# Optimization experiments

Hardware: AMD Instinct MI355X
Metric: run time of the kernel (lower is better)

Reference implementation:

```python
import jax, jax.numpy as jnp
import numpy as np

INPUT_DIM, OUTPUT_DIM = 128, 256
FPS_FACTOR, KNN = 14, 10


def fps(pcd, K):
    """Farthest point sampling. pcd: [B,N,3] -> (points [B,K,3], indices [B,K]).
    Deterministic start at index 0 (pytorch3d uses first/random point)."""
    B, N, _ = pcd.shape
    first = jnp.zeros((B,), jnp.int32)
    init_d = jnp.full((B, N), 1e10, pcd.dtype)

    def step(carry, _):
        dists, last = carry
        lp = jnp.take_along_axis(pcd, last[:, None, None], axis=1)  # [B,1,3]
        d = jnp.sum((pcd - lp) ** 2, axis=-1)                        # [B,N]
        dists = jnp.minimum(dists, d)
        nxt = jnp.argmax(dists, axis=-1).astype(jnp.int32)
        return (dists, nxt), nxt

    (_, _), rest = jax.lax.scan(step, (init_d, first), None, length=K - 1)
    idx = jnp.concatenate([first[None, :], rest], axis=0).T  # [B,K]
    pts = jnp.take_along_axis(pcd, idx[..., None], axis=1)   # [B,K,3]
    return pts, idx


def knn_idx(q, p, k):
    """q:[B,Q,3], p:[B,N,3] -> nearest-neighbor indices [B,Q,k] (squared L2)."""
    d = (jnp.sum(q * q, -1)[:, :, None] + jnp.sum(p * p, -1)[:, None, :]
         - 2.0 * jnp.einsum('bqc,bnc->bqn', q, p))
    _, idx = jax.lax.top_k(-d, k)
    return idx


_bgather = jax.vmap(lambda a, i: a[i])  # per-batch fancy gather


def setup_inputs() -> dict:
    key = jax.random.key(0)
    k1, k2, k3, k4, k5 = jax.random.split(key, 5)
    B, N = 4, 16384
    tgt = jax.random.normal(k1, (B, N, INPUT_DIM), jnp.float32)
    pcd_x = jax.random.normal(k2, (B, N, 3), jnp.float32)
    pcd_v = jax.random.normal(k3, (B, N, 3, 3), jnp.float32)
    W = jax.random.normal(k4, (INPUT_DIM, OUTPUT_DIM), jnp.float32) / np.sqrt(INPUT_DIM)
    b = jax.random.normal(k5, (OUTPUT_DIM,), jnp.float32) * 0.01
    return {"tgt": tgt, "pcd_x": pcd_x, "pcd_v": pcd_v, "W": W, "b": b}


def reference(tgt, pcd_x, pcd_v, W, b):
    B, N, D = tgt.shape
    n_out = N // FPS_FACTOR
    out_pcd_x, out_indices = fps(pcd_x, n_out)          # [B,n_out,3], [B,n_out]
    nn = knn_idx(out_pcd_x, pcd_x, KNN)                 # [B,n_out,k]

    knn_pcd = _bgather(pcd_x, nn)                       # [B,n_out,k,3]
    query_f = jnp.take_along_axis(tgt, out_indices[..., None], axis=1)  # [B,n_out,D]
    query_c = out_pcd_x
    query_v = _bgather(pcd_v, out_indices)              # [B,n_out,V,3]
    key_f = _bgather(tgt, nn)                           # [B,n_out,k,D]
    key_c = knn_pcd
    key_v = _bgather(pcd_v, nn)                         # [B,n_out,k,V,3]

    # flatten (B*n_out) super-point groups, project features
    _query_f = query_f.reshape(-1, D)[:, None, :] @ W + b          # [B*n_out,1,O]
    _key_f = key_f.reshape(-1, KNN, D) @ W + b                     # [B*n_out,k,O]
    del _key_f, key_c, key_v  # consumed by the (identity stand-in) transformer

    # NOTE: URSATransformer stand-in = identity on the projected query features
    out_query_f = _query_f.reshape(B, n_out, OUTPUT_DIM)
    return out_query_f, query_c, query_v
```

## Files before the change

### kernel.cpp

```cpp
#include <hip/hip_runtime.h>

constexpr int B_   = 4;
constexpr int N_   = 16384;
constexpr int NOUT = 1170;
constexpr int D_   = 128;
constexpr int O_   = 256;

typedef float f32x2 __attribute__((ext_vector_type(2)));
typedef unsigned long long u64;

template <int CTRL>
__device__ __forceinline__ float dpp_fmax(float x) {
  int yi = __builtin_amdgcn_update_dpp(__float_as_int(x), __float_as_int(x),
                                       CTRL, 0xF, 0xF, false);
  return fmaxf(x, __int_as_float(yi));
}

constexpr int TPB_FPS = 512;
constexpr int PPT   = N_ / TPB_FPS;
constexpr int NPAIR = PPT / 2;
constexpr int NW    = TPB_FPS / 64;

__global__ __launch_bounds__(TPB_FPS)
__attribute__((amdgpu_waves_per_eu(2, 2)))
void fps_kernel(const float* __restrict__ pcd_x,
                int* __restrict__ sel,
                float* __restrict__ out_c) {
  const int b = blockIdx.x, t = threadIdx.x;
  const float* __restrict__ P = pcd_x + (size_t)b * N_ * 3;
  const int base = t * PPT;
  const int lane = t & 63;

  f32x2 x[NPAIR], y[NPAIR], z[NPAIR], dm[NPAIR];
#pragma unroll
  for (int k = 0; k < NPAIR; ++k) {
    const int p0 = base + 2 * k;
    x[k]  = f32x2{P[p0 * 3 + 0], P[p0 * 3 + 3]};
    y[k]  = f32x2{P[p0 * 3 + 1], P[p0 * 3 + 4]};
    z[k]  = f32x2{P[p0 * 3 + 2], P[p0 * 3 + 5]};
    dm[k] = f32x2{1e10f, 1e10f};
  }

  __shared__ float2 s_pair[2][NW];

  float lx = P[0], ly = P[1], lz = P[2];
  if (t == 0) {
    sel[b * NOUT + 0] = 0;
    out_c[((size_t)b * NOUT + 0) * 3 + 0] = lx;
    out_c[((size_t)b * NOUT + 0) * 3 + 1] = ly;
    out_c[((size_t)b * NOUT + 0) * 3 + 2] = lz;
  }

  for (int step = 1; step < NOUT; ++step) {
    const int par = step & 1;

    asm volatile("" : "+v"(x[0]), "+v"(x[1]), "+v"(x[2]), "+v"(x[3]),
                      "+v"(x[4]), "+v"(x[5]), "+v"(x[6]), "+v"(x[7]),
                      "+v"(x[8]), "+v"(x[9]), "+v"(x[10]), "+v"(x[11]),
                      "+v"(x[12]), "+v"(x[13]), "+v"(x[14]), "+v"(x[15]));
    asm volatile("" : "+v"(y[0]), "+v"(y[1]), "+v"(y[2]), "+v"(y[3]),
                      "+v"(y[4]), "+v"(y[5]), "+v"(y[6]), "+v"(y[7]),
                      "+v"(y[8]), "+v"(y[9]), "+v"(y[10]), "+v"(y[11]),
                      "+v"(y[12]), "+v"(y[13]), "+v"(y[14]), "+v"(y[15]));
    asm volatile("" : "+v"(z[0]), "+v"(z[1]), "+v"(z[2]), "+v"(z[3]),
                      "+v"(z[4]), "+v"(z[5]), "+v"(z[6]), "+v"(z[7]),
                      "+v"(z[8]), "+v"(z[9]), "+v"(z[10]), "+v"(z[11]),
                      "+v"(z[12]), "+v"(z[13]), "+v"(z[14]), "+v"(z[15]));

    const f32x2 lxx = {lx, lx}, lyy = {ly, ly}, lzz = {lz, lz};
    f32x2 bv2 = {-1.0f, -1.0f};
    {
#pragma clang fp contract(off)
#pragma unroll
      for (int k = 0; k < NPAIR; ++k) {
        const f32x2 dx = x[k] - lxx;
        const f32x2 dy = y[k] - lyy;
        const f32x2 dz = z[k] - lzz;
        const f32x2 s  = (dx * dx + dy * dy) + dz * dz;
        f32x2 nd;
        nd.x = fminf(dm[k].x, s.x);
        nd.y = fminf(dm[k].y, s.y);
        dm[k] = nd;
        bv2.x = fmaxf(bv2.x, nd.x);
        bv2.y = fmaxf(bv2.y, nd.y);
      }
    }
    const float bv = fmaxf(bv2.x, bv2.y);

    float wm = bv;
    wm = dpp_fmax<0xB1>(wm);
    wm = dpp_fmax<0x4E>(wm);
    wm = dpp_fmax<0x141>(wm);
    wm = dpp_fmax<0x140>(wm);
    wm = dpp_fmax<0x142>(wm);
    wm = dpp_fmax<0x143>(wm);
    const float wmax =
        __int_as_float(__builtin_amdgcn_readlane(__float_as_int(wm), 63));

    int bi = 0;
#pragma unroll
    for (int k = NPAIR - 1; k >= 0; --k) {
      if (dm[k].y == bv) bi = base + 2 * k + 1;
      if (dm[k].x == bv) bi = base + 2 * k;
    }

    const u64 mask = __ballot(bv == wmax);
    const int flane = __builtin_ctzll(mask);
    if (lane == flane) {
      float2 pr;
      pr.x = wmax;
      pr.y = __int_as_float(bi);
      s_pair[par][t >> 6] = pr;
    }
    __syncthreads();

    const float2 e = s_pair[par][lane & (NW - 1)];
    float gv = e.x;
    gv = dpp_fmax<0xB1>(gv);
    gv = dpp_fmax<0x4E>(gv);
    gv = dpp_fmax<0x141>(gv);
    const u64 m2 = __ballot(e.x == gv);
    const int ww = __builtin_ctzll(m2);
    int ri = __builtin_amdgcn_readlane(__float_as_int(e.y), ww);

    lx = P[ri * 3 + 0];
    ly = P[ri * 3 + 1];
    lz = P[ri * 3 + 2];
    if (t == 0) {
      sel[b * NOUT + step] = ri;
      out_c[((size_t)b * NOUT + step) * 3 + 0] = lx;
      out_c[((size_t)b * NOUT + step) * 3 + 1] = ly;
      out_c[((size_t)b * NOUT + step) * 3 + 2] = lz;
    }
  }
}

constexpr int TPB_PROJ = 256;
constexpr int RPB = 4;

__global__ __launch_bounds__(TPB_PROJ)
void proj_kernel(const float* __restrict__ tgt,
                 const float* __restrict__ pcd_v,
                 const float* __restrict__ W,
                 const float* __restrict__ bias,
                 const int* __restrict__ sel,
                 float* __restrict__ out_f,
                 float* __restrict__ out_v) {
  const int t = threadIdx.x;
  const int row0 = blockIdx.x * RPB;
  __shared__ float sA[RPB * D_];
  __shared__ int   sIdx[RPB];
  if (t < RPB) {
    const int row = row0 + t;
    const int b = row / NOUT;
    sIdx[t] = b * N_ + sel[row];
  }
  __syncthreads();
#pragma unroll
  for (int l = 0; l < RPB * D_ / TPB_PROJ; ++l) {
    const int e = t + l * TPB_PROJ;
    const int r = e >> 7, k = e & (D_ - 1);
    sA[e] = tgt[(size_t)sIdx[r] * D_ + k];
  }
  __syncthreads();
  float acc0 = 0.f, acc1 = 0.f, acc2 = 0.f, acc3 = 0.f;
#pragma unroll 8
  for (int k = 0; k < D_; ++k) {
    const float w = W[k * O_ + t];
    acc0 = fmaf(sA[0 * D_ + k], w, acc0);
    acc1 = fmaf(sA[1 * D_ + k], w, acc1);
    acc2 = fmaf(sA[2 * D_ + k], w, acc2);
    acc3 = fmaf(sA[3 * D_ + k], w, acc3);
  }
  const float bb = bias[t];
  out_f[(size_t)(row0 + 0) * O_ + t] = acc0 + bb;
  out_f[(size_t)(row0 + 1) * O_ + t] = acc1 + bb;
  out_f[(size_t)(row0 + 2) * O_ + t] = acc2 + bb;
  out_f[(size_t)(row0 + 3) * O_ + t] = acc3 + bb;
  if (t < RPB * 9) {
    const int r = t / 9, e = t - r * 9;
    out_v[(size_t)(row0 + r) * 9 + e] = pcd_v[(size_t)sIdx[r] * 9 + e];
  }
}

extern "C" void kernel_launch(void* const* d_in, const int* in_sizes, int n_in,
                              void* d_out, int out_size, void* d_ws, size_t ws_size,
                              hipStream_t stream) {
  const float* tgt   = (const float*)d_in[0];
  const float* pcd_x = (const float*)d_in[1];
  const float* pcd_v = (const float*)d_in[2];
  const float* W     = (const float*)d_in[3];
  const float* bias  = (const float*)d_in[4];

  float* out   = (float*)d_out;
  float* out_f = out;
  float* out_c = out + (size_t)B_ * NOUT * O_;
  float* out_v = out_c + (size_t)B_ * NOUT * 3;

  int* sel = (int*)d_ws;

  hipLaunchKernelGGL(fps_kernel, dim3(B_), dim3(TPB_FPS), 0, stream,
                     pcd_x, sel, out_c);
  hipLaunchKernelGGL(proj_kernel, dim3(B_ * NOUT / RPB), dim3(TPB_PROJ), 0, stream,
                     tgt, pcd_v, W, bias, sel, out_f, out_v);
}
```

Measured before the change: 1.920 ms.

## Widen FPS block to 1024 threads with x/y in LDS and index-min reductions

```diff
diff --git a/kernel.cpp b/kernel.cpp
--- a/kernel.cpp
+++ b/kernel.cpp
@@ -15,33 +15,44 @@
                                        CTRL, 0xF, 0xF, false);
   return fmaxf(x, __int_as_float(yi));
 }
-
-constexpr int TPB_FPS = 512;
-constexpr int PPT   = N_ / TPB_FPS;
-constexpr int NPAIR = PPT / 2;
+template <int CTRL>
+__device__ __forceinline__ int dpp_imin(int x) {
+  int y = __builtin_amdgcn_update_dpp(x, x, CTRL, 0xF, 0xF, false);
+  return y < x ? y : x;
+}
+
+constexpr int TPB_FPS = 1024;
+constexpr int PPT   = 16;
+constexpr int NPR   = 8;
 constexpr int NW    = TPB_FPS / 64;
-
-__global__ __launch_bounds__(TPB_FPS)
-__attribute__((amdgpu_waves_per_eu(2, 2)))
+constexpr size_t LDS_BYTES = (size_t)2 * N_ * 4 + NW * 8 + 16;
+
+__global__ __launch_bounds__(TPB_FPS, 1)
 void fps_kernel(const float* __restrict__ pcd_x,
                 int* __restrict__ sel,
                 float* __restrict__ out_c) {
+  extern __shared__ float smem[];
+  float*  xs     = smem;
+  float*  ys     = smem + N_;
+  float2* s_pair = (float2*)(smem + 2 * N_);
+  float*  s_z    = (float*)(s_pair + NW);
+
   const int b = blockIdx.x, t = threadIdx.x;
+  const int lane = t & 63, w = t >> 6;
   const float* __restrict__ P = pcd_x + (size_t)b * N_ * 3;
-  const int base = t * PPT;
-  const int lane = t & 63;
-
-  f32x2 x[NPAIR], y[NPAIR], z[NPAIR], dm[NPAIR];
-#pragma unroll
-  for (int k = 0; k < NPAIR; ++k) {
-    const int p0 = base + 2 * k;
-    x[k]  = f32x2{P[p0 * 3 + 0], P[p0 * 3 + 3]};
-    y[k]  = f32x2{P[p0 * 3 + 1], P[p0 * 3 + 4]};
-    z[k]  = f32x2{P[p0 * 3 + 2], P[p0 * 3 + 5]};
-    dm[k] = f32x2{1e10f, 1e10f};
-  }
-
-  __shared__ float2 s_pair[2][NW];
+
+  f32x2 zs[NPR], dm[NPR];
+#pragma unroll
+  for (int j = 0; j < NPR; ++j) {
+    const int p0 = 2 * t + j * 2048;
+    const float x0 = P[p0 * 3 + 0], y0 = P[p0 * 3 + 1], z0 = P[p0 * 3 + 2];
+    const float x1 = P[p0 * 3 + 3], y1 = P[p0 * 3 + 4], z1 = P[p0 * 3 + 5];
+    *reinterpret_cast<f32x2*>(&xs[p0]) = f32x2{x0, x1};
+    *reinterpret_cast<f32x2*>(&ys[p0]) = f32x2{y0, y1};
+    zs[j] = f32x2{z0, z1};
+    dm[j] = f32x2{1e10f, 1e10f};
+  }
+  __syncthreads();
 
   float lx = P[0], ly = P[1], lz = P[2];
   if (t == 0) {
@@ -52,40 +63,33 @@
   }
 
   for (int step = 1; step < NOUT; ++step) {
-    const int par = step & 1;
-
-    asm volatile("" : "+v"(x[0]), "+v"(x[1]), "+v"(x[2]), "+v"(x[3]),
-                      "+v"(x[4]), "+v"(x[5]), "+v"(x[6]), "+v"(x[7]),
-                      "+v"(x[8]), "+v"(x[9]), "+v"(x[10]), "+v"(x[11]),
-                      "+v"(x[12]), "+v"(x[13]), "+v"(x[14]), "+v"(x[15]));
-    asm volatile("" : "+v"(y[0]), "+v"(y[1]), "+v"(y[2]), "+v"(y[3]),
-                      "+v"(y[4]), "+v"(y[5]), "+v"(y[6]), "+v"(y[7]),
-                      "+v"(y[8]), "+v"(y[9]), "+v"(y[10]), "+v"(y[11]),
-                      "+v"(y[12]), "+v"(y[13]), "+v"(y[14]), "+v"(y[15]));
-    asm volatile("" : "+v"(z[0]), "+v"(z[1]), "+v"(z[2]), "+v"(z[3]),
-                      "+v"(z[4]), "+v"(z[5]), "+v"(z[6]), "+v"(z[7]),
-                      "+v"(z[8]), "+v"(z[9]), "+v"(z[10]), "+v"(z[11]),
-                      "+v"(z[12]), "+v"(z[13]), "+v"(z[14]), "+v"(z[15]));
-
-    const f32x2 lxx = {lx, lx}, lyy = {ly, ly}, lzz = {lz, lz};
-    f32x2 bv2 = {-1.0f, -1.0f};
+    const float nx = __int_as_float(__float_as_int(lx) ^ 0x80000000);
+    const float ny = __int_as_float(__float_as_int(ly) ^ 0x80000000);
+    const float nz = __int_as_float(__float_as_int(lz) ^ 0x80000000);
+    const f32x2 nlx = {nx, nx}, nly = {ny, ny}, nlz = {nz, nz};
+
+    f32x2 bvv = {-1.0f, -1.0f};
     {
 #pragma clang fp contract(off)
 #pragma unroll
-      for (int k = 0; k < NPAIR; ++k) {
-        const f32x2 dx = x[k] - lxx;
-        const f32x2 dy = y[k] - lyy;
-        const f32x2 dz = z[k] - lzz;
+      for (int j = 0; j < NPR; ++j) {
+        const int p0 = 2 * t + j * 2048;
+        const f32x2 xv = *reinterpret_cast<const f32x2*>(&xs[p0]);
+        const f32x2 yv = *reinterpret_cast<const f32x2*>(&ys[p0]);
+        const f32x2 dx = xv + nlx;
+        const f32x2 dy = yv + nly;
+        const f32x2 dz = zs[j] + nlz;
         const f32x2 s  = (dx * dx + dy * dy) + dz * dz;
-        f32x2 nd;
-        nd.x = fminf(dm[k].x, s.x);
-        nd.y = fminf(dm[k].y, s.y);
-        dm[k] = nd;
-        bv2.x = fmaxf(bv2.x, nd.x);
-        bv2.y = fmaxf(bv2.y, nd.y);
+        dm[j] = __builtin_elementwise_min(dm[j], s);
+        bvv   = __builtin_elementwise_max(bvv, dm[j]);
       }
     }
-    const float bv = fmaxf(bv2.x, bv2.y);
+    const float bv = fmaxf(bvv.x, bvv.y);
+
+    asm volatile("" : "+v"(zs[0]), "+v"(zs[1]), "+v"(zs[2]), "+v"(zs[3]),
+                      "+v"(zs[4]), "+v"(zs[5]), "+v"(zs[6]), "+v"(zs[7]));
+    asm volatile("" : "+v"(dm[0]), "+v"(dm[1]), "+v"(dm[2]), "+v"(dm[3]),
+                      "+v"(dm[4]), "+v"(dm[5]), "+v"(dm[6]), "+v"(dm[7]));
 
     float wm = bv;
     wm = dpp_fmax<0xB1>(wm);
@@ -97,35 +101,46 @@
     const float wmax =
         __int_as_float(__builtin_amdgcn_readlane(__float_as_int(wm), 63));
 
-    int bi = 0;
-#pragma unroll
-    for (int k = NPAIR - 1; k >= 0; --k) {
-      if (dm[k].y == bv) bi = base + 2 * k + 1;
-      if (dm[k].x == bv) bi = base + 2 * k;
-    }
-
-    const u64 mask = __ballot(bv == wmax);
-    const int flane = __builtin_ctzll(mask);
-    if (lane == flane) {
-      float2 pr;
-      pr.x = wmax;
-      pr.y = __int_as_float(bi);
-      s_pair[par][t >> 6] = pr;
-    }
+    int bi = 0x7fffffff;
+#pragma unroll
+    for (int j = NPR - 1; j >= 0; --j) {
+      if (dm[j].y == bv) bi = 2 * t + j * 2048 + 1;
+      if (dm[j].x == bv) bi = 2 * t + j * 2048;
+    }
+    int mi = (bv == wmax) ? bi : 0x7fffffff;
+    mi = dpp_imin<0xB1>(mi);
+    mi = dpp_imin<0x4E>(mi);
+    mi = dpp_imin<0x141>(mi);
+    mi = dpp_imin<0x140>(mi);
+    mi = dpp_imin<0x142>(mi);
+    mi = dpp_imin<0x143>(mi);
+    const int widx = __builtin_amdgcn_readlane(mi, 63);
+
+    if (lane == 0) s_pair[w] = make_float2(wmax, __int_as_float(widx));
     __syncthreads();
 
-    const float2 e = s_pair[par][lane & (NW - 1)];
+    const float2 e = s_pair[lane & (NW - 1)];
     float gv = e.x;
     gv = dpp_fmax<0xB1>(gv);
     gv = dpp_fmax<0x4E>(gv);
     gv = dpp_fmax<0x141>(gv);
-    const u64 m2 = __ballot(e.x == gv);
-    const int ww = __builtin_ctzll(m2);
-    int ri = __builtin_amdgcn_readlane(__float_as_int(e.y), ww);
-
-    lx = P[ri * 3 + 0];
-    ly = P[ri * 3 + 1];
-    lz = P[ri * 3 + 2];
+    gv = dpp_fmax<0x140>(gv);
+    int m2 = (e.x == gv) ? __float_as_int(e.y) : 0x7fffffff;
+    m2 = dpp_imin<0xB1>(m2);
+    m2 = dpp_imin<0x4E>(m2);
+    m2 = dpp_imin<0x141>(m2);
+    m2 = dpp_imin<0x140>(m2);
+    const int ri = __builtin_amdgcn_readfirstlane(m2);
+
+    if (t == ((ri & 2047) >> 1)) {
+      const int oj = ri >> 11, oh = ri & 1;
+      s_z[0] = oh ? zs[oj].y : zs[oj].x;
+    }
+    __syncthreads();
+
+    lx = xs[ri];
+    ly = ys[ri];
+    lz = s_z[0];
     if (t == 0) {
       sel[b * NOUT + step] = ri;
       out_c[((size_t)b * NOUT + step) * 3 + 0] = lx;
@@ -199,7 +214,7 @@
 
   int* sel = (int*)d_ws;
 
-  hipLaunchKernelGGL(fps_kernel, dim3(B_), dim3(TPB_FPS), 0, stream,
+  hipLaunchKernelGGL(fps_kernel, dim3(B_), dim3(TPB_FPS), LDS_BYTES, stream,
                      pcd_x, sel, out_c);
   hipLaunchKernelGGL(proj_kernel, dim3(B_ * NOUT / RPB), dim3(TPB_PROJ), 0, stream,
                      tgt, pcd_v, W, bias, sel, out_f, out_v);
```

Measured after the change: 2.126 ms. 1.11x slower.
